# Performance work log

Hardware: AMD Instinct MI355X
Metric: run time of the kernel (lower is better)

Reference implementation:

```python
import jax, jax.numpy as jnp
import numpy as np

THETA = 10000.0
D_K = 128
MAX_SEQ_LEN = 4096


def setup_inputs() -> dict:
    key = jax.random.key(0)
    k1, k2 = jax.random.split(key)
    x = jax.random.normal(k1, (4, 32, 4096, D_K), dtype=jnp.float32)
    token_positions = jax.random.randint(k2, (4, 32, 4096), 0, MAX_SEQ_LEN, dtype=jnp.int64)
    return {"x": x, "token_positions": token_positions}


def reference(x, token_positions):
    # Original builds a block-diagonal [max_seq_len, d_k, d_k] rotation matrix r with
    # 2x2 blocks [[cos, -sin], [sin, cos]] for angle theta_ik = pos / theta**(2k/d_k),
    # then computes out[row] = sum_col r[pos, row, col] * x[col].
    # Off-block entries are exactly zero, so this equals the standard pairwise rotation:
    #   out[2k]   = cos*x[2k] - sin*x[2k+1]
    #   out[2k+1] = sin*x[2k] + cos*x[2k+1]
    k = jnp.arange(D_K // 2, dtype=jnp.float32)
    inv_freq = THETA ** (-2.0 * k / D_K)                      # [d_k/2]
    pos = token_positions.astype(jnp.float32)                 # [... seq]
    angles = pos[..., None] * inv_freq                        # [... seq d_k/2]
    cos, sin = jnp.cos(angles), jnp.sin(angles)
    xe = x[..., 0::2]                                         # even channels
    xo = x[..., 1::2]                                         # odd channels
    out_e = cos * xe - sin * xo
    out_o = sin * xe + cos * xo
    # interleave back: [..., seq, d_k/2, 2] -> [..., seq, d_k]
    out = jnp.stack([out_e, out_o], axis=-1).reshape(x.shape)
    return out
```

## Files before the change

### kernel.cpp

```cpp
#include <hip/hip_runtime.h>


#define BLOCK 256

__global__ __launch_bounds__(BLOCK) void rope_kernel(
    const float4* __restrict__ x,
    const int* __restrict__ pos,
    float4* __restrict__ out,
    int n_f4)
{
    int tid = blockIdx.x * BLOCK + threadIdx.x;
    if (tid >= n_f4) return;

    int row = tid >> 5;
    int j   = tid & 31;

    float p = (float)pos[row];
    float4 v = x[tid];

    const float c = -0.2076205059304601f;
    float k0 = (float)(2 * j);
    float a0 = p * exp2f(k0 * c);
    float a1 = p * exp2f((k0 + 1.0f) * c);

    float s0, c0, s1, c1;
    sincosf(a0, &s0, &c0);
    sincosf(a1, &s1, &c1);

    float4 r;
    r.x = c0 * v.x - s0 * v.y;
    r.y = s0 * v.x + c0 * v.y;
    r.z = c1 * v.z - s1 * v.w;
    r.w = s1 * v.z + c1 * v.w;
    out[tid] = r;
}

extern "C" void kernel_launch(void* const* d_in, const int* in_sizes, int n_in,
                              void* d_out, int out_size, void* d_ws, size_t ws_size,
                              hipStream_t stream) {
    const float4* x  = (const float4*)d_in[0];
    const int* pos   = (const int*)d_in[1];
    float4* out      = (float4*)d_out;

    int n_f4 = out_size / 4;
    int blocks = (n_f4 + BLOCK - 1) / BLOCK;
    rope_kernel<<<blocks, BLOCK, 0, stream>>>(x, pos, out, n_f4);
}
```

Before: 414.6 us.

## Precompute cos/sin table per position and use grid-stride nontemporal main kernel

```diff
diff --git a/kernel.cpp b/kernel.cpp
--- a/kernel.cpp
+++ b/kernel.cpp
@@ -2,47 +2,60 @@
 
 
 #define BLOCK 256
+#define MAX_POS 4096
+#define DK2 64
 
-__global__ __launch_bounds__(BLOCK) void rope_kernel(
-    const float4* __restrict__ x,
+typedef float vf4 __attribute__((ext_vector_type(4)));
+
+__global__ __launch_bounds__(BLOCK) void rope_table(float2* __restrict__ tab)
+{
+    int tid = blockIdx.x * BLOCK + threadIdx.x;
+    int p = tid >> 6;
+    int k = tid & 63;
+    const float c = -0.2076205059304601f;
+    float a = (float)p * exp2f((float)k * c);
+    float s, co;
+    sincosf(a, &s, &co);
+    tab[tid] = make_float2(co, s);
+}
+
+__global__ __launch_bounds__(BLOCK) void rope_main(
+    const vf4* __restrict__ x,
     const int* __restrict__ pos,
-    float4* __restrict__ out,
+    const vf4* __restrict__ tab,
+    vf4* __restrict__ out,
     int n_f4)
 {
-    int tid = blockIdx.x * BLOCK + threadIdx.x;
-    if (tid >= n_f4) return;
+    int stride = gridDim.x * BLOCK;
+    for (int tid = blockIdx.x * BLOCK + threadIdx.x; tid < n_f4; tid += stride) {
+        int row = tid >> 5;
+        int j   = tid & 31;
 
-    int row = tid >> 5;
-    int j   = tid & 31;
+        int p = pos[row];
+        vf4 t = tab[p * 32 + j];
+        vf4 v = __builtin_nontemporal_load(&x[tid]);
 
-    float p = (float)pos[row];
-    float4 v = x[tid];
-
-    const float c = -0.2076205059304601f;
-    float k0 = (float)(2 * j);
-    float a0 = p * exp2f(k0 * c);
-    float a1 = p * exp2f((k0 + 1.0f) * c);
-
-    float s0, c0, s1, c1;
-    sincosf(a0, &s0, &c0);
-    sincosf(a1, &s1, &c1);
-
-    float4 r;
-    r.x = c0 * v.x - s0 * v.y;
-    r.y = s0 * v.x + c0 * v.y;
-    r.z = c1 * v.z - s1 * v.w;
-    r.w = s1 * v.z + c1 * v.w;
-    out[tid] = r;
+        vf4 r;
+        r.x = t.x * v.x - t.y * v.y;
+        r.y = t.y * v.x + t.x * v.y;
+        r.z = t.z * v.z - t.w * v.w;
+        r.w = t.w * v.z + t.z * v.w;
+        __builtin_nontemporal_store(r, &out[tid]);
+    }
 }
 
 extern "C" void kernel_launch(void* const* d_in, const int* in_sizes, int n_in,
                               void* d_out, int out_size, void* d_ws, size_t ws_size,
                               hipStream_t stream) {
-    const float4* x  = (const float4*)d_in[0];
-    const int* pos   = (const int*)d_in[1];
-    float4* out      = (float4*)d_out;
+    const vf4* x   = (const vf4*)d_in[0];
+    const int* pos = (const int*)d_in[1];
+    vf4* out       = (vf4*)d_out;
+    float2* tab    = (float2*)d_ws;
+
+    rope_table<<<(MAX_POS * DK2) / BLOCK, BLOCK, 0, stream>>>(tab);
 
     int n_f4 = out_size / 4;
     int blocks = (n_f4 + BLOCK - 1) / BLOCK;
-    rope_kernel<<<blocks, BLOCK, 0, stream>>>(x, pos, out, n_f4);
+    if (blocks > 2048) blocks = 2048;
+    rope_main<<<blocks, BLOCK, 0, stream>>>(x, pos, (const vf4*)tab, out, n_f4);
 }
```

Result: slower. 429.5 us (+3.6%).
